# Optimization experiments

Hardware: AMD Instinct MI355X
Metric: run time of the kernel (lower is better)

## Reference

```python
import jax, jax.numpy as jnp
import numpy as np

IN_DIM, DIM, G, B = 512, 1024, 16, 4096

def _gelu(x):
    return jax.nn.gelu(x, approximate=False)  # torch nn.GELU default = exact erf


def setup_inputs() -> dict:
    key = jax.random.key(0)
    ks = jax.random.split(key, 11)
    sc_in = 1.0 / np.sqrt(IN_DIM)
    sc_d = 1.0 / np.sqrt(DIM)
    return {
        "x": jax.random.normal(ks[0], (B, IN_DIM), dtype=jnp.float32),
        "genre": jax.random.randint(ks[1], (B,), 0, G),
        # shared MLP params
        "W1": jax.random.uniform(ks[2], (IN_DIM, DIM), jnp.float32, -sc_in, sc_in),
        "b1": jax.random.uniform(ks[3], (DIM,), jnp.float32, -sc_in, sc_in),
        "W2": jax.random.uniform(ks[4], (DIM, DIM), jnp.float32, -sc_d, sc_d),
        "b2": jax.random.uniform(ks[5], (DIM,), jnp.float32, -sc_d, sc_d),
        # unshared (per-genre) MLP params, stacked over experts
        "Wa": jax.random.uniform(ks[6], (G, DIM, DIM), jnp.float32, -sc_d, sc_d),
        "ba": jax.random.uniform(ks[7], (G, DIM), jnp.float32, -sc_d, sc_d),
        "Wb": jax.random.uniform(ks[8], (G, DIM, DIM), jnp.float32, -sc_d, sc_d),
        "bb": jax.random.uniform(ks[9], (G, DIM), jnp.float32, -sc_d, sc_d),
    }


def reference(x, genre, W1, b1, W2, b2, Wa, ba, Wb, bb):
    # shared trunk: Linear -> GELU -> Linear -> GELU
    s = _gelu(_gelu(x @ W1 + b1) @ W2 + b2)          # [B, D]
    # dense per-genre expert branches (faithful to original: compute all, then gather)
    h = _gelu(jnp.einsum('bd,gde->bge', s, Wa) + ba[None, :, :])  # [B, G, D]
    out_all = jnp.einsum('bgd,gde->bge', h, Wb) + bb[None, :, :]  # [B, G, D]
    # gather each sample's own genre branch
    return jnp.take_along_axis(out_all, genre[:, None, None], axis=1)[:, 0, :]  # [B, D]
```

## Files before the change

### kernel.cpp

```cpp
#include <hip/hip_runtime.h>
#include <hip/hip_bf16.h>
#include <math.h>

#define BATCH 4096
#define INDIM 512
#define NDIM  1024
#define NG    16

typedef __bf16 bf16_t;
typedef __bf16 bf16x8 __attribute__((ext_vector_type(8)));
typedef float  f32x4  __attribute__((ext_vector_type(4)));
typedef unsigned int u32;
typedef unsigned int u32x4 __attribute__((ext_vector_type(4)));

__device__ __forceinline__ float gelu_exact(float v) {
    return 0.5f * v * (1.0f + erff(v * 0.70710678118654752440f));
}

__device__ __forceinline__ void gload_lds16(const void* g, void* l) {
    __builtin_amdgcn_global_load_lds((const __attribute__((address_space(1))) void*)g,
                                     (__attribute__((address_space(3))) void*)l,
                                     16, 0, 0);
}

__global__ __launch_bounds__(256)
void build_perm_kernel(const int* __restrict__ genre,
                       int* __restrict__ perm,
                       int* __restrict__ offsets ) {
    __shared__ int cc[64][NG];
    __shared__ int gtot[NG];
    __shared__ int goff[NG];
    const int t = threadIdx.x;
    for (int i = t; i < 64 * NG; i += 256) (&cc[0][0])[i] = 0;
    __syncthreads();
    if (t < 64) {
        #pragma unroll 1
        for (int i = 0; i < 64; ++i) {
            int g = genre[t * 64 + i] & (NG - 1);
            cc[t][g] += 1;
        }
    }
    __syncthreads();
    if (t < NG) {
        int s = 0;
        #pragma unroll 1
        for (int c = 0; c < 64; ++c) { int v = cc[c][t]; cc[c][t] = s; s += v; }
        gtot[t] = s;
    }
    __syncthreads();
    if (t == 0) {
        int s = 0;
        for (int g = 0; g < NG; ++g) { goff[g] = s; offsets[g] = s; s += gtot[g]; }
        offsets[NG] = s;
    }
    __syncthreads();
    if (t < 64) {
        #pragma unroll 1
        for (int i = 0; i < 64; ++i) {
            int b = t * 64 + i;
            int g = genre[b] & (NG - 1);
            int pos = goff[g] + cc[t][g];
            cc[t][g] += 1;
            perm[pos] = b;
        }
    }
}

__global__ __launch_bounds__(256)
void convert_x_kernel(const float* __restrict__ src, bf16_t* __restrict__ dst) {
    const int i = (blockIdx.x * 256 + threadIdx.x) * 8;
    float4 a = *(const float4*)&src[i];
    float4 b = *(const float4*)&src[i + 4];
    bf16x8 w;
    w[0] = (bf16_t)a.x; w[1] = (bf16_t)a.y; w[2] = (bf16_t)a.z; w[3] = (bf16_t)a.w;
    w[4] = (bf16_t)b.x; w[5] = (bf16_t)b.y; w[6] = (bf16_t)b.z; w[7] = (bf16_t)b.w;
    *(bf16x8*)&dst[i] = w;
}

__device__ __forceinline__ u32 pkbf(float a, float b) {
    union { bf16_t h[2]; u32 v; } x;
    x.h[0] = (bf16_t)a; x.h[1] = (bf16_t)b;
    return x.v;
}

__global__ __launch_bounds__(256)
void transpose_w_kernel(const float* __restrict__ src, bf16_t* __restrict__ dst,
                        int K, int N) {
    __shared__ u32 T[64][17];
    const int k0 = blockIdx.x * 32;
    const int n0 = blockIdx.y * 64;
    const size_t slab = (size_t)blockIdx.z * (size_t)K * (size_t)N;
    src += slab;
    dst += slab;
    const int t = threadIdx.x;
    {
        const int kr = (t >> 4) * 2;
        const int nc = (t & 15) * 4;
        const float* p0 = src + (size_t)(k0 + kr) * N + n0 + nc;
        const float* p1 = p0 + N;
        float4 r0 = *(const float4*)p0;
        float4 r1 = *(const float4*)p1;
        const int kp = t >> 4;
        T[nc + 0][kp] = pkbf(r0.x, r1.x);
        T[nc + 1][kp] = pkbf(r0.y, r1.y);
        T[nc + 2][kp] = pkbf(r0.z, r1.z);
        T[nc + 3][kp] = pkbf(r0.w, r1.w);
    }
    __syncthreads();
    {
        const int n = t >> 2;
        const int c = t & 3;
        u32x4 v;
        v.x = T[n][c * 4 + 0];
        v.y = T[n][c * 4 + 1];
        v.z = T[n][c * 4 + 2];
        v.w = T[n][c * 4 + 3];
        *(u32x4*)((char*)dst + ((size_t)(n0 + n) * K + k0 + c * 8) * 2) = v;
    }
}

template<bool EXPERT, bool GATHER_A, bool GELU_OUT, bool SCATTER_OUT, bool OUT_BF16>
__global__ __launch_bounds__(1024, 4)
void gemm128_kernel(const bf16_t* __restrict__ A,
                    const bf16_t* __restrict__ Bt,
                    const float* __restrict__ bias,
                    void* __restrict__ Cout,
                    int K,
                    const int* __restrict__ perm,
                    const int* __restrict__ offsets) {
    constexpr int N = NDIM;
    __shared__ bf16_t As[2][128 * 64];
    __shared__ bf16_t Bs[2][128 * 64];

    const int n0 = blockIdx.y * 128;
    int m0 = 0, mloc0 = 0, count = 1 << 30, gbase = 0;
    const bf16_t* Bp = Bt;
    const float* biasp = bias;

    if constexpr (EXPERT) {
        const int bx = blockIdx.x;
        int g = 0, accum = 0, cnt = 0;
        for (; g < NG; ++g) {
            cnt = offsets[g + 1] - offsets[g];
            int nt = (cnt + 127) >> 7;
            if (bx < accum + nt) break;
            accum += nt;
        }
        if (g >= NG) return;
        count = cnt;
        mloc0 = (bx - accum) * 128;
        gbase = offsets[g];
        m0 = gbase + mloc0;
        Bp = Bt + (size_t)g * N * NDIM;
        biasp = bias + g * N;
    } else {
        m0 = blockIdx.x * 128;
    }

    const int tid  = threadIdx.x;
    const int wave = tid >> 6;
    const int lane = tid & 63;
    const int l15  = lane & 15;
    const int l16  = lane >> 4;
    const int wr   = wave >> 2;
    const int wc   = wave & 3;

    const int srow   = tid >> 3;
    const int srcoff = (((tid & 7) ^ ((tid >> 3) & 7)) * 16);
    int arow;
    if constexpr (EXPERT) {
        int rcl = mloc0 + srow;
        if (rcl >= count) rcl = count - 1;
        arow = GATHER_A ? perm[gbase + rcl] : (gbase + rcl);
    } else {
        arow = m0 + srow;
    }
    const char* aptr = (const char*)(A + (size_t)arow * K) + srcoff;
    const char* bptr = (const char*)(Bp + (size_t)(n0 + srow) * K) + srcoff;

    f32x4 acc[2][2];
    #pragma unroll
    for (int m = 0; m < 2; ++m)
        #pragma unroll
        for (int n = 0; n < 2; ++n)
            acc[m][n] = (f32x4){0.f, 0.f, 0.f, 0.f};

    const int nsteps = K >> 6;
    const int w1024 = wave * 1024;

    auto stage = [&](int buf, int t) {
        const size_t ko = (size_t)t * 128;
        gload_lds16(aptr + ko, (char*)&As[buf][0] + w1024);
        gload_lds16(bptr + ko, (char*)&Bs[buf][0] + w1024);
    };

    stage(0, 0);
    int cur = 0;
    for (int t = 0; t < nsteps; ++t) {
        if (t + 1 < nsteps) {
            stage(cur ^ 1, t + 1);
            asm volatile("s_waitcnt vmcnt(2)" ::: "memory");
        } else {
            asm volatile("s_waitcnt vmcnt(0)" ::: "memory");
        }
        asm volatile("s_barrier" ::: "memory");

        #pragma unroll
        for (int kk = 0; kk < 2; ++kk) {
            bf16x8 a[2], b[2];
            #pragma unroll
            for (int m = 0; m < 2; ++m) {
                const int row = wr * 32 + m * 16 + l15;
                const int chunk = (kk * 4 + l16) ^ (lane & 7);
                a[m] = *(const bf16x8*)&As[cur][row * 64 + chunk * 8];
            }
            #pragma unroll
            for (int n = 0; n < 2; ++n) {
                const int row = wc * 32 + n * 16 + l15;
                const int chunk = (kk * 4 + l16) ^ (lane & 7);
                b[n] = *(const bf16x8*)&Bs[cur][row * 64 + chunk * 8];
            }
            #pragma unroll
            for (int m = 0; m < 2; ++m)
                #pragma unroll
                for (int n = 0; n < 2; ++n)
                    acc[m][n] = __builtin_amdgcn_mfma_f32_16x16x32_bf16(a[m], b[n], acc[m][n], 0, 0, 0);
        }
        asm volatile("s_barrier" ::: "memory");
        cur ^= 1;
    }

    #pragma unroll
    for (int n = 0; n < 2; ++n) {
        const int col = n0 + wc * 32 + n * 16 + l15;
        const float bv = biasp[col];
        #pragma unroll
        for (int m = 0; m < 2; ++m) {
            #pragma unroll
            for (int r = 0; r < 4; ++r) {
                const int row_local = wr * 32 + m * 16 + l16 * 4 + r;
                if constexpr (EXPERT) {
                    if (mloc0 + row_local >= count) continue;
                }
                float v = acc[m][n][r] + bv;
                if constexpr (GELU_OUT) v = gelu_exact(v);
                int orow = m0 + row_local;
                if constexpr (SCATTER_OUT) orow = perm[orow];
                if constexpr (OUT_BF16)
                    ((bf16_t*)Cout)[(size_t)orow * N + col] = (bf16_t)v;
                else
                    ((float*)Cout)[(size_t)orow * N + col] = v;
            }
        }
    }
}

extern "C" void kernel_launch(void* const* d_in, const int* in_sizes, int n_in,
                              void* d_out, int out_size, void* d_ws, size_t ws_size,
                              hipStream_t stream) {
    const float* x     = (const float*)d_in[0];
    const int*   genre = (const int*)  d_in[1];
    const float* W1    = (const float*)d_in[2];
    const float* b1    = (const float*)d_in[3];
    const float* W2    = (const float*)d_in[4];
    const float* b2    = (const float*)d_in[5];
    const float* Wa    = (const float*)d_in[6];
    const float* ba    = (const float*)d_in[7];
    const float* Wb    = (const float*)d_in[8];
    const float* bb    = (const float*)d_in[9];
    float* out = (float*)d_out;

    char* ws = (char*)d_ws;
    const size_t MB = 1 << 20;
    bf16_t* W1t = (bf16_t*)(ws);
    bf16_t* W2t = (bf16_t*)(ws + 1 * MB);
    bf16_t* Wat = (bf16_t*)(ws + 3 * MB);
    bf16_t* Wbt = (bf16_t*)(ws + 35 * MB);
    bf16_t* xb  = (bf16_t*)(ws + 67 * MB);
    bf16_t* s1b = (bf16_t*)(ws + 71 * MB);
    bf16_t* sb  = (bf16_t*)(ws + 79 * MB);
    int*    perm    = (int*)(ws + 87 * MB);
    int*    offsets = (int*)(ws + 87 * MB + 65536);
    bf16_t* hb = s1b;

    build_perm_kernel<<<1, 256, 0, stream>>>(genre, perm, offsets);
    convert_x_kernel<<<BATCH * INDIM / (256 * 8), 256, 0, stream>>>(x, xb);
    transpose_w_kernel<<<dim3(INDIM / 32, NDIM / 64, 1),  256, 0, stream>>>(W1, W1t, INDIM, NDIM);
    transpose_w_kernel<<<dim3(NDIM / 32, NDIM / 64, 1),   256, 0, stream>>>(W2, W2t, NDIM, NDIM);
    transpose_w_kernel<<<dim3(NDIM / 32, NDIM / 64, NG),  256, 0, stream>>>(Wa, Wat, NDIM, NDIM);
    transpose_w_kernel<<<dim3(NDIM / 32, NDIM / 64, NG),  256, 0, stream>>>(Wb, Wbt, NDIM, NDIM);

    gemm128_kernel<false, false, true, false, true><<<dim3(32, 8), 1024, 0, stream>>>(
        xb, W1t, b1, s1b, INDIM, nullptr, nullptr);
    gemm128_kernel<false, false, true, false, true><<<dim3(32, 8), 1024, 0, stream>>>(
        s1b, W2t, b2, sb, NDIM, nullptr, nullptr);
    gemm128_kernel<true, true, true, false, true><<<dim3(48, 8), 1024, 0, stream>>>(
        sb, Wat, ba, hb, NDIM, perm, offsets);
    gemm128_kernel<true, false, false, true, false><<<dim3(48, 8), 1024, 0, stream>>>(
        hb, Wbt, bb, out, NDIM, perm, offsets);
}
```

Baseline: 149.2 us.

## Shrink GEMM M-tile to 64 rows with 512 threads and merge expert transposes

The GEMM kernel moves from a 128x128 tile with 1024 threads to a 64x128 tile with 512 threads. Each thread now stages one A chunk and two B chunks, and the wait count is adjusted to match. This doubles the block count, which should fill more CUs and cut padding waste on ragged expert groups, at the cost of less reuse of the B tile per block. The two expert weight transposes are also merged into one launch over 32 z-slices to save a kernel launch.

```diff
diff --git a/kernel.cpp b/kernel.cpp
--- a/kernel.cpp
+++ b/kernel.cpp
@@ -83,16 +83,10 @@
     return x.v;
 }
 
-__global__ __launch_bounds__(256)
-void transpose_w_kernel(const float* __restrict__ src, bf16_t* __restrict__ dst,
-                        int K, int N) {
+__device__ __forceinline__ void transpose_tile(const float* __restrict__ src,
+                                               bf16_t* __restrict__ dst,
+                                               int K, int N, int k0, int n0, int t) {
     __shared__ u32 T[64][17];
-    const int k0 = blockIdx.x * 32;
-    const int n0 = blockIdx.y * 64;
-    const size_t slab = (size_t)blockIdx.z * (size_t)K * (size_t)N;
-    src += slab;
-    dst += slab;
-    const int t = threadIdx.x;
     {
         const int kr = (t >> 4) * 2;
         const int nc = (t & 15) * 4;
@@ -119,17 +113,35 @@
     }
 }
 
+__global__ __launch_bounds__(256)
+void transpose_w_kernel(const float* __restrict__ src, bf16_t* __restrict__ dst,
+                        int K, int N) {
+    const size_t slab = (size_t)blockIdx.z * (size_t)K * (size_t)N;
+    transpose_tile(src + slab, dst + slab, K, N, blockIdx.x * 32, blockIdx.y * 64,
+                   threadIdx.x);
+}
+
+__global__ __launch_bounds__(256)
+void transpose_w2_kernel(const float* __restrict__ srcA, bf16_t* __restrict__ dstA,
+                         const float* __restrict__ srcB, bf16_t* __restrict__ dstB) {
+    const int z = blockIdx.z;
+    const size_t slab = (size_t)(z & 15) * NDIM * NDIM;
+    const float* s = (z < 16 ? srcA : srcB) + slab;
+    bf16_t*      d = (z < 16 ? dstA : dstB) + slab;
+    transpose_tile(s, d, NDIM, NDIM, blockIdx.x * 32, blockIdx.y * 64, threadIdx.x);
+}
+
 template<bool EXPERT, bool GATHER_A, bool GELU_OUT, bool SCATTER_OUT, bool OUT_BF16>
-__global__ __launch_bounds__(1024, 4)
-void gemm128_kernel(const bf16_t* __restrict__ A,
-                    const bf16_t* __restrict__ Bt,
-                    const float* __restrict__ bias,
-                    void* __restrict__ Cout,
-                    int K,
-                    const int* __restrict__ perm,
-                    const int* __restrict__ offsets) {
+__global__ __launch_bounds__(512, 6)
+void gemm64_kernel(const bf16_t* __restrict__ A,
+                   const bf16_t* __restrict__ Bt,
+                   const float* __restrict__ bias,
+                   void* __restrict__ Cout,
+                   int K,
+                   const int* __restrict__ perm,
+                   const int* __restrict__ offsets) {
     constexpr int N = NDIM;
-    __shared__ bf16_t As[2][128 * 64];
+    __shared__ bf16_t As[2][64 * 64];
     __shared__ bf16_t Bs[2][128 * 64];
 
     const int n0 = blockIdx.y * 128;
@@ -142,19 +154,19 @@
         int g = 0, accum = 0, cnt = 0;
         for (; g < NG; ++g) {
             cnt = offsets[g + 1] - offsets[g];
-            int nt = (cnt + 127) >> 7;
+            int nt = (cnt + 63) >> 6;
             if (bx < accum + nt) break;
             accum += nt;
         }
         if (g >= NG) return;
         count = cnt;
-        mloc0 = (bx - accum) * 128;
+        mloc0 = (bx - accum) * 64;
         gbase = offsets[g];
         m0 = gbase + mloc0;
         Bp = Bt + (size_t)g * N * NDIM;
         biasp = bias + g * N;
     } else {
-        m0 = blockIdx.x * 128;
+        m0 = blockIdx.x * 64;
     }
 
     const int tid  = threadIdx.x;
@@ -175,8 +187,9 @@
     } else {
         arow = m0 + srow;
     }
-    const char* aptr = (const char*)(A + (size_t)arow * K) + srcoff;
-    const char* bptr = (const char*)(Bp + (size_t)(n0 + srow) * K) + srcoff;
+    const char* aptr  = (const char*)(A + (size_t)arow * K) + srcoff;
+    const char* bptr0 = (const char*)(Bp + (size_t)(n0 + srow) * K) + srcoff;
+    const char* bptr1 = (const char*)(Bp + (size_t)(n0 + 64 + srow) * K) + srcoff;
 
     f32x4 acc[2][2];
     #pragma unroll
@@ -186,12 +199,13 @@
             acc[m][n] = (f32x4){0.f, 0.f, 0.f, 0.f};
 
     const int nsteps = K >> 6;
-    const int w1024 = wave * 1024;
+    const int t16 = tid * 16;
 
     auto stage = [&](int buf, int t) {
         const size_t ko = (size_t)t * 128;
-        gload_lds16(aptr + ko, (char*)&As[buf][0] + w1024);
-        gload_lds16(bptr + ko, (char*)&Bs[buf][0] + w1024);
+        gload_lds16(aptr  + ko, (char*)&As[buf][0] + t16);
+        gload_lds16(bptr0 + ko, (char*)&Bs[buf][0] + t16);
+        gload_lds16(bptr1 + ko, (char*)&Bs[buf][0] + 8192 + t16);
     };
 
     stage(0, 0);
@@ -199,7 +213,7 @@
     for (int t = 0; t < nsteps; ++t) {
         if (t + 1 < nsteps) {
             stage(cur ^ 1, t + 1);
-            asm volatile("s_waitcnt vmcnt(2)" ::: "memory");
+            asm volatile("s_waitcnt vmcnt(3)" ::: "memory");
         } else {
             asm volatile("s_waitcnt vmcnt(0)" ::: "memory");
         }
@@ -285,17 +299,17 @@
 
     build_perm_kernel<<<1, 256, 0, stream>>>(genre, perm, offsets);
     convert_x_kernel<<<BATCH * INDIM / (256 * 8), 256, 0, stream>>>(x, xb);
-    transpose_w_kernel<<<dim3(INDIM / 32, NDIM / 64, 1),  256, 0, stream>>>(W1, W1t, INDIM, NDIM);
-    transpose_w_kernel<<<dim3(NDIM / 32, NDIM / 64, 1),   256, 0, stream>>>(W2, W2t, NDIM, NDIM);
-    transpose_w_kernel<<<dim3(NDIM / 32, NDIM / 64, NG),  256, 0, stream>>>(Wa, Wat, NDIM, NDIM);
-    transpose_w_kernel<<<dim3(NDIM / 32, NDIM / 64, NG),  256, 0, stream>>>(Wb, Wbt, NDIM, NDIM);
-
-    gemm128_kernel<false, false, true, false, true><<<dim3(32, 8), 1024, 0, stream>>>(
+    transpose_w_kernel<<<dim3(INDIM / 32, NDIM / 64, 1), 256, 0, stream>>>(W1, W1t, INDIM, NDIM);
+    transpose_w_kernel<<<dim3(NDIM / 32, NDIM / 64, 1),  256, 0, stream>>>(W2, W2t, NDIM, NDIM);
+    transpose_w2_kernel<<<dim3(NDIM / 32, NDIM / 64, 2 * NG), 256, 0, stream>>>(
+        Wa, Wat, Wb, Wbt);
+
+    gemm64_kernel<false, false, true, false, true><<<dim3(64, 8), 512, 0, stream>>>(
         xb, W1t, b1, s1b, INDIM, nullptr, nullptr);
-    gemm128_kernel<false, false, true, false, true><<<dim3(32, 8), 1024, 0, stream>>>(
+    gemm64_kernel<false, false, true, false, true><<<dim3(64, 8), 512, 0, stream>>>(
         s1b, W2t, b2, sb, NDIM, nullptr, nullptr);
-    gemm128_kernel<true, true, true, false, true><<<dim3(48, 8), 1024, 0, stream>>>(
+    gemm64_kernel<true, true, true, false, true><<<dim3(80, 8), 512, 0, stream>>>(
         sb, Wat, ba, hb, NDIM, perm, offsets);
-    gemm128_kernel<true, false, false, true, false><<<dim3(48, 8), 1024, 0, stream>>>(
+    gemm64_kernel<true, false, false, true, false><<<dim3(80, 8), 512, 0, stream>>>(
         hb, Wbt, bb, out, NDIM, perm, offsets);
 }
```

Result: slower. 156.7 us (+5.0%).
